# Performance work log

Measured on AMD Instinct MI355X. Metric: run time of the kernel, lower is better.

Reference implementation:

```python
import jax, jax.numpy as jnp
import numpy as np

B, T, C = 2, 4096, 2048
HS = 64          # module head size (r_k, kk normalize, GroupNorm groups)
H = C // HS      # 32
NK = 16          # kernel head dim (RUN_CUDA_RWKV7g views heads of 16)
HK = C // NK     # 128
LORA = 8
GN_EPS = 0.00064

def setup_inputs() -> dict:
    key = jax.random.key(0)
    ks = jax.random.split(key, 32)
    rn = lambda k, shape, s=1.0: jax.random.normal(k, shape, dtype=jnp.float32) * s
    sW = 0.5 / (C ** 0.5)
    return {
        'x': rn(ks[0], (B, T, C)),
        'v_first': rn(ks[1], (B, T, C)),
        'x_r': jax.random.uniform(ks[2], (1, 1, C)), 'x_w': jax.random.uniform(ks[3], (1, 1, C)),
        'x_k': jax.random.uniform(ks[4], (1, 1, C)), 'x_v': jax.random.uniform(ks[5], (1, 1, C)),
        'x_a': jax.random.uniform(ks[6], (1, 1, C)), 'x_g': jax.random.uniform(ks[7], (1, 1, C)),
        'w0': rn(ks[8], (1, 1, C), 0.5) - 3.0,
        'w1': rn(ks[9], (C, LORA), 0.02), 'w2': rn(ks[10], (LORA, C), 0.1),
        'a0': rn(ks[11], (1, 1, C), 0.1),
        'a1': rn(ks[12], (C, LORA), 0.02), 'a2': rn(ks[13], (LORA, C), 0.1),
        'v0': rn(ks[14], (1, 1, C), 0.1) + 0.73,
        'v1': rn(ks[15], (C, LORA), 0.02), 'v2': rn(ks[16], (LORA, C), 0.1),
        'g1': rn(ks[17], (C, LORA), 0.02), 'g2': rn(ks[18], (LORA, C), 0.1),
        'k_k': rn(ks[19], (1, 1, C), 0.05) + 0.71,
        'k_a': rn(ks[20], (1, 1, C), 0.05) + 1.02,
        'r_k': rn(ks[21], (H, HS), 0.02) - 0.04,
        'Wr': rn(ks[22], (C, C), sW), 'Wk': rn(ks[23], (C, C), 0.1 * sW),
        'Wv': rn(ks[24], (C, C), sW), 'Wo': rn(ks[25], (C, C), sW),
        'ln_g': jnp.ones((C,), jnp.float32), 'ln_b': jnp.zeros((C,), jnp.float32),
    }

def _rwkv7_scan(r, w, k, v, a, b):
    # each (B,T,C) -> heads (T,B,HK,NK); recurrence: S = S*exp(-exp(w)) + (S@a)b^T + v k^T; y = S@r
    th = lambda t: t.reshape(B, T, HK, NK).transpose(1, 0, 2, 3)
    rs, ws, ks_, vs, as_, bs = map(th, (r, w, k, v, a, b))
    decay = jnp.exp(-jnp.exp(ws))
    def step(S, inp):
        d_t, r_t, k_t, v_t, a_t, b_t = inp
        sa = jnp.einsum('bhij,bhj->bhi', S, a_t)                      # old state @ a
        S = (S * d_t[:, :, None, :]
             + sa[..., None] * b_t[:, :, None, :]
             + v_t[..., None] * k_t[:, :, None, :])
        y = jnp.einsum('bhij,bhj->bhi', S, r_t)
        return S, y
    S0 = jnp.zeros((B, HK, NK, NK), jnp.float32)
    _, ys = jax.lax.scan(step, S0, (decay, rs, ks_, vs, as_, bs))
    return ys.transpose(1, 0, 2, 3).reshape(B, T, C)

def reference(x, v_first, x_r, x_w, x_k, x_v, x_a, x_g,
              w0, w1, w2, a0, a1, a2, v0, v1, v2, g1, g2,
              k_k, k_a, r_k, Wr, Wk, Wv, Wo, ln_g, ln_b):
    xx = jnp.pad(x, ((0, 0), (1, 0), (0, 0)))[:, :T] - x   # token shift
    xr = x + xx * x_r; xw = x + xx * x_w; xk_ = x + xx * x_k
    xv = x + xx * x_v; xa = x + xx * x_a; xg_ = x + xx * x_g
    r = xr @ Wr.T
    w = -jax.nn.softplus(-(w0 + jnp.tanh(xw @ w1) @ w2)) - 0.5
    k = xk_ @ Wk.T
    v = xv @ Wv.T
    v_mix = jax.nn.sigmoid(v0 + (xv @ v1) @ v2)            # layer_id != 0 branch
    v = v + (v_first - v) * v_mix
    a = jax.nn.sigmoid(a0 + (xa @ a1) @ a2)
    g = jax.nn.sigmoid(xg_ @ g1) @ g2
    kk = k * k_k
    kk4 = kk.reshape(B, T, H, HS)
    kk = (kk4 / jnp.maximum(jnp.linalg.norm(kk4, axis=-1, keepdims=True), 1e-8)).reshape(B, T, C)
    k = k * (1 + (a - 1) * k_a)
    o = _rwkv7_scan(r, w, k, v, -kk, kk * a)
    # GroupNorm(H groups, eps=6.4e-4) over B*T rows
    og = o.reshape(B * T, H, HS)
    mu = og.mean(-1, keepdims=True)
    var = og.var(-1, keepdims=True)
    o = (((og - mu) / jnp.sqrt(var + GN_EPS)).reshape(B * T, C) * ln_g + ln_b).reshape(B, T, C)
    rh = r.reshape(B, T, H, HS); kh = k.reshape(B, T, H, HS); vh = v.reshape(B, T, H, HS)
    o = o + ((rh * kh * r_k).sum(-1, keepdims=True) * vh).reshape(B, T, C)
    out = (o * g) @ Wo.T
    return (out, v_first)
```

## Files before the change

### kernel.cpp

```cpp
#include <hip/hip_runtime.h>

#define T_LEN 4096
#define C_DIM 2048
#define REC 224
#define CH 64
#define CHB (CH * REC)

typedef __attribute__((ext_vector_type(4))) float f32x4;
typedef __attribute__((ext_vector_type(8))) __bf16 bf16x8;
typedef __attribute__((ext_vector_type(8))) unsigned short u16x8;
typedef __attribute__((ext_vector_type(4))) unsigned int u32x4;
typedef __attribute__((ext_vector_type(2))) unsigned int u32x2;
typedef unsigned short u16;
typedef unsigned int u32;

typedef __attribute__((address_space(1))) const void* as1cv;
typedef __attribute__((address_space(3))) void* as3v;

__device__ __forceinline__ void gld16(const void* g, void* l) {
  __builtin_amdgcn_global_load_lds((as1cv)g, (as3v)l, 16, 0, 0);
}

__device__ __forceinline__ u16 f2bf(float f) {
  union { float f; unsigned u; } x; x.f = f;
  return (u16)((x.u + 0x7fffu + ((x.u >> 16) & 1u)) >> 16);
}
__device__ __forceinline__ float bflo(unsigned u) {
  union { unsigned u; float f; } x; x.u = u << 16; return x.f;
}
__device__ __forceinline__ float bfhi(unsigned u) {
  union { unsigned u; float f; } x; x.u = u & 0xffff0000u; return x.f;
}
__device__ __forceinline__ float red16(float x) {
  int a;
  a = __builtin_amdgcn_update_dpp(0, __builtin_bit_cast(int, x), 0xB1, 0xF, 0xF, true);
  x += __builtin_bit_cast(float, a);
  a = __builtin_amdgcn_update_dpp(0, __builtin_bit_cast(int, x), 0x4E, 0xF, 0xF, true);
  x += __builtin_bit_cast(float, a);
  a = __builtin_amdgcn_update_dpp(0, __builtin_bit_cast(int, x), 0x124, 0xF, 0xF, true);
  x += __builtin_bit_cast(float, a);
  a = __builtin_amdgcn_update_dpp(0, __builtin_bit_cast(int, x), 0x128, 0xF, 0xF, true);
  x += __builtin_bit_cast(float, a);
  return x;
}
__device__ __forceinline__ f32x4 red16v(f32x4 v) {
  v[0] = red16(v[0]); v[1] = red16(v[1]);
  v[2] = red16(v[2]); v[3] = red16(v[3]);
  return v;
}

__global__ __launch_bounds__(256)
void conv_bf16_k(const float* __restrict__ s0, const float* __restrict__ s1,
                 const float* __restrict__ s2, const float* __restrict__ s3,
                 u16* __restrict__ d0) {
  const float* s = (blockIdx.y == 0) ? s0 : (blockIdx.y == 1) ? s1
                   : (blockIdx.y == 2) ? s2 : s3;
  u16* d = d0 + (size_t)blockIdx.y * 4194304;
  int i = (blockIdx.x * 256 + threadIdx.x) * 8;
  f32x4 a = *(const f32x4*)(s + i);
  f32x4 b = *(const f32x4*)(s + i + 4);
  u16x8 o;
  o[0] = f2bf(a[0]); o[1] = f2bf(a[1]); o[2] = f2bf(a[2]); o[3] = f2bf(a[3]);
  o[4] = f2bf(b[0]); o[5] = f2bf(b[1]); o[6] = f2bf(b[2]); o[7] = f2bf(b[3]);
  *(u16x8*)(d + i) = o;
}

__global__ __launch_bounds__(256)
void trans_lora_k(const float* __restrict__ w1, const float* __restrict__ a1,
                  const float* __restrict__ v1, const float* __restrict__ g1,
                  float* __restrict__ wt) {
  const float* s = (blockIdx.y == 0) ? w1 : (blockIdx.y == 1) ? a1
                   : (blockIdx.y == 2) ? v1 : g1;
  float* d = wt + (size_t)blockIdx.y * (8 * C_DIM);
  int c = blockIdx.x * 256 + threadIdx.x;
  f32x4 lo = *(const f32x4*)(s + c * 8);
  f32x4 hi = *(const f32x4*)(s + c * 8 + 4);
  d[0 * C_DIM + c] = lo[0]; d[1 * C_DIM + c] = lo[1];
  d[2 * C_DIM + c] = lo[2]; d[3 * C_DIM + c] = lo[3];
  d[4 * C_DIM + c] = hi[0]; d[5 * C_DIM + c] = hi[1];
  d[6 * C_DIM + c] = hi[2]; d[7 * C_DIM + c] = hi[3];
}

__global__ __launch_bounds__(256)
void mix_lora_k(const float* __restrict__ x,
                const float* __restrict__ xrw, const float* __restrict__ xww,
                const float* __restrict__ xkw, const float* __restrict__ xvw,
                const float* __restrict__ xaw, const float* __restrict__ xgw,
                const float* __restrict__ wt,
                u16* __restrict__ xr_bf, u16* __restrict__ xk_bf,
                u16* __restrict__ xv_bf, float* __restrict__ lora8) {
  const int pr = blockIdx.x * 2;
  const int t0 = pr & (T_LEN - 1);
  const int tid = threadIdx.x;
  const float* xr0 = x + (size_t)pr * C_DIM;
  const float* xr1 = xr0 + C_DIM;
  float wl0[8], al0[8], vl0[8], gl0[8];
  float wl1[8], al1[8], vl1[8], gl1[8];
  #pragma unroll
  for (int l = 0; l < 8; ++l) {
    wl0[l] = 0.f; al0[l] = 0.f; vl0[l] = 0.f; gl0[l] = 0.f;
    wl1[l] = 0.f; al1[l] = 0.f; vl1[l] = 0.f; gl1[l] = 0.f;
  }
  #pragma unroll
  for (int ii = 0; ii < 8; ++ii) {
    const int c = ii * 256 + tid;
    float x0 = xr0[c], x1 = xr1[c];
    float xm = t0 ? xr0[c - C_DIM] : 0.f;
    float dx0 = xm - x0;
    float dx1 = x0 - x1;
    float mr = xrw[c], mw = xww[c], mk = xkw[c];
    float mv = xvw[c], ma = xaw[c], mg = xgw[c];
    float xw0 = fmaf(dx0, mw, x0), xw1 = fmaf(dx1, mw, x1);
    float xa0 = fmaf(dx0, ma, x0), xa1 = fmaf(dx1, ma, x1);
    float xv0 = fmaf(dx0, mv, x0), xv1 = fmaf(dx1, mv, x1);
    float xg0 = fmaf(dx0, mg, x0), xg1 = fmaf(dx1, mg, x1);
    xr_bf[(size_t)pr * C_DIM + c] = f2bf(fmaf(dx0, mr, x0));
    xr_bf[(size_t)(pr + 1) * C_DIM + c] = f2bf(fmaf(dx1, mr, x1));
    xk_bf[(size_t)pr * C_DIM + c] = f2bf(fmaf(dx0, mk, x0));
    xk_bf[(size_t)(pr + 1) * C_DIM + c] = f2bf(fmaf(dx1, mk, x1));
    xv_bf[(size_t)pr * C_DIM + c] = f2bf(xv0);
    xv_bf[(size_t)(pr + 1) * C_DIM + c] = f2bf(xv1);
    #pragma unroll
    for (int l = 0; l < 8; ++l) {
      float tw = wt[l * C_DIM + c];
      float ta = wt[16384 + l * C_DIM + c];
      float tv = wt[32768 + l * C_DIM + c];
      float tg = wt[49152 + l * C_DIM + c];
      wl0[l] = fmaf(xw0, tw, wl0[l]); wl1[l] = fmaf(xw1, tw, wl1[l]);
      al0[l] = fmaf(xa0, ta, al0[l]); al1[l] = fmaf(xa1, ta, al1[l]);
      vl0[l] = fmaf(xv0, tv, vl0[l]); vl1[l] = fmaf(xv1, tv, vl1[l]);
      gl0[l] = fmaf(xg0, tg, gl0[l]); gl1[l] = fmaf(xg1, tg, gl1[l]);
    }
  }
  __shared__ __attribute__((aligned(16))) float red2[2][16][32];
  const int row = tid >> 4;
  f32x4 t0v, t1v;
  #pragma unroll
  for (int half = 0; half < 2; ++half) {
    float* wl = half ? wl1 : wl0;
    float* al = half ? al1 : al0;
    float* vl = half ? vl1 : vl0;
    float* gl = half ? gl1 : gl0;
    t0v = red16v((f32x4){wl[0], wl[1], wl[2], wl[3]});
    t1v = red16v((f32x4){wl[4], wl[5], wl[6], wl[7]});
    if ((tid & 15) == 0) {
      *(f32x4*)&red2[half][row][0] = t0v; *(f32x4*)&red2[half][row][4] = t1v;
    }
    t0v = red16v((f32x4){al[0], al[1], al[2], al[3]});
    t1v = red16v((f32x4){al[4], al[5], al[6], al[7]});
    if ((tid & 15) == 0) {
      *(f32x4*)&red2[half][row][8] = t0v; *(f32x4*)&red2[half][row][12] = t1v;
    }
    t0v = red16v((f32x4){vl[0], vl[1], vl[2], vl[3]});
    t1v = red16v((f32x4){vl[4], vl[5], vl[6], vl[7]});
    if ((tid & 15) == 0) {
      *(f32x4*)&red2[half][row][16] = t0v; *(f32x4*)&red2[half][row][20] = t1v;
    }
    t0v = red16v((f32x4){gl[0], gl[1], gl[2], gl[3]});
    t1v = red16v((f32x4){gl[4], gl[5], gl[6], gl[7]});
    if ((tid & 15) == 0) {
      *(f32x4*)&red2[half][row][24] = t0v; *(f32x4*)&red2[half][row][28] = t1v;
    }
  }
  __syncthreads();
  if (tid < 64) {
    const int rw = tid >> 5, idx = tid & 31;
    float s = 0.f;
    #pragma unroll
    for (int r = 0; r < 16; ++r) s += red2[rw][r][idx];
    int mat = idx >> 3;
    if (mat == 0) s = tanhf(s);
    else if (mat == 3) s = 1.f / (1.f + expf(-s));
    lora8[(size_t)(pr + rw) * 32 + idx] = s;
  }
}

__device__ __forceinline__ int swzslot(int row, int slot) {
  return slot ^ ((row >> 1) & 3);
}

__global__ __launch_bounds__(512)
void gemm8_k(const u16* __restrict__ A0, const u16* __restrict__ A1,
             const u16* __restrict__ A2, const u16* __restrict__ B0,
             const u16* __restrict__ B1, const u16* __restrict__ B2,
             char* __restrict__ out, int pmode) {
  extern __shared__ __attribute__((aligned(16))) char smem[];
  u16* Asm = (u16*)smem;
  u16* Bsm = (u16*)(smem + 65536);
  const int z = blockIdx.z;
  const u16* A = (z == 0) ? A0 : (z == 1) ? A1 : A2;
  const u16* Bw = (z == 0) ? B0 : (z == 1) ? B1 : B2;
  const int sbase = (z == 0) ? 4 : (z == 1) ? 6 : 192;
  const int sstr = (z == 2) ? 2 : 8;
  const int tid = threadIdx.x;
  const int wv = tid >> 6, ln = tid & 63;
  const int wr = wv >> 2, wc = wv & 3;
  const int bid = blockIdx.x + (blockIdx.y << 3);
  const int sw = (bid & 7) * 32 + (bid >> 3);
  const int row0 = (sw >> 3) * 256, col0 = (sw & 7) * 256;
  const int s_rw = tid >> 2;
  const int s_slotL = (tid & 3) ^ ((s_rw >> 1) & 3);
  int aoff[8], boff[4];
  #pragma unroll
  for (int m = 0; m < 8; ++m) {
    int row = wr * 128 + m * 16 + (ln & 15);
    aoff[m] = row * 32 + swzslot(row, ln >> 4) * 8;
  }
  #pragma unroll
  for (int n = 0; n < 4; ++n) {
    int row = wc * 64 + n * 16 + (ln & 15);
    boff[n] = row * 32 + swzslot(row, ln >> 4) * 8;
  }
  f32x4 acc[8][4];
  #pragma unroll
  for (int m = 0; m < 8; ++m)
    #pragma unroll
    for (int n = 0; n < 4; ++n) acc[m][n] = (f32x4){0.f, 0.f, 0.f, 0.f};

  auto abase = [&](int db, int kh) -> u16* { return Asm + (db * 2 + kh) * 8192; };
  auto bbase = [&](int db, int kh) -> u16* { return Bsm + (db * 2 + kh) * 8192; };
  auto stage1 = [&](const u16* src, int baserow, u16* lbase, int kh, int skt, int rblk) {
    const u16* g = src + (size_t)(baserow + rblk * 128 + s_rw) * 2048
                   + skt * 64 + kh * 32 + s_slotL * 8;
    gld16(g, lbase + rblk * 4096 + wv * 512);
  };
  auto khblockA = [&](int db, int skt, bool doStage) {
    const u16* Ab = abase(db, 0);
    const u16* Bb = bbase(db, 0);
    const int sdb = skt & 1;
    bf16x8 bf[4], af[4];
    #pragma unroll
    for (int n = 0; n < 4; ++n) bf[n] = *(const bf16x8*)(Bb + boff[n]);
    #pragma unroll
    for (int m = 0; m < 4; ++m) af[m] = *(const bf16x8*)(Ab + aoff[m]);
    if (doStage) {
      stage1(A, row0, abase(sdb, 0), 0, skt, 0);
      stage1(A, row0, abase(sdb, 0), 0, skt, 1);
      stage1(Bw, col0, bbase(sdb, 0), 0, skt, 0);
      stage1(Bw, col0, bbase(sdb, 0), 0, skt, 1);
    }
    __builtin_amdgcn_s_setprio(1);
    #pragma unroll
    for (int m = 0; m < 4; ++m)
      #pragma unroll
      for (int n = 0; n < 4; ++n)
        acc[m][n] = __builtin_amdgcn_mfma_f32_16x16x32_bf16(af[m], bf[n], acc[m][n], 0, 0, 0);
    __builtin_amdgcn_s_setprio(0);
    #pragma unroll
    for (int m = 0; m < 4; ++m) af[m] = *(const bf16x8*)(Ab + aoff[4 + m]);
    if (doStage) {
      stage1(A, row0, abase(sdb, 1), 1, skt, 0);
      stage1(A, row0, abase(sdb, 1), 1, skt, 1);
      stage1(Bw, col0, bbase(sdb, 1), 1, skt, 0);
      stage1(Bw, col0, bbase(sdb, 1), 1, skt, 1);
    }
    __builtin_amdgcn_s_setprio(1);
    #pragma unroll
    for (int m = 0; m < 4; ++m)
      #pragma unroll
      for (int n = 0; n < 4; ++n)
        acc[4 + m][n] = __builtin_amdgcn_mfma_f32_16x16x32_bf16(af[m], bf[n], acc[4 + m][n], 0, 0, 0);
    __builtin_amdgcn_s_setprio(0);
  };
  auto khblockB = [&](int db) {
    const u16* Ab = abase(db, 1);
    const u16* Bb = bbase(db, 1);
    bf16x8 bf[4], af[4];
    #pragma unroll
    for (int n = 0; n < 4; ++n) bf[n] = *(const bf16x8*)(Bb + boff[n]);
    #pragma unroll
    for (int m = 0; m < 4; ++m) af[m] = *(const bf16x8*)(Ab + aoff[m]);
    __builtin_amdgcn_s_setprio(1);
    #pragma unroll
    for (int m = 0; m < 4; ++m)
      #pragma unroll
      for (int n = 0; n < 4; ++n)
        acc[m][n] = __builtin_amdgcn_mfma_f32_16x16x32_bf16(af[m], bf[n], acc[m][n], 0, 0, 0);
    __builtin_amdgcn_s_setprio(0);
    #pragma unroll
    for (int m = 0; m < 4; ++m) af[m] = *(const bf16x8*)(Ab + aoff[4 + m]);
    __builtin_amdgcn_s_setprio(1);
    #pragma unroll
    for (int m = 0; m < 4; ++m)
      #pragma unroll
      for (int n = 0; n < 4; ++n)
        acc[4 + m][n] = __builtin_amdgcn_mfma_f32_16x16x32_bf16(af[m], bf[n], acc[4 + m][n], 0, 0, 0);
    __builtin_amdgcn_s_setprio(0);
  };

  stage1(A, row0, abase(0, 0), 0, 0, 0); stage1(A, row0, abase(0, 0), 0, 0, 1);
  stage1(Bw, col0, bbase(0, 0), 0, 0, 0); stage1(Bw, col0, bbase(0, 0), 0, 0, 1);
  stage1(A, row0, abase(0, 1), 1, 0, 0); stage1(A, row0, abase(0, 1), 1, 0, 1);
  stage1(Bw, col0, bbase(0, 1), 1, 0, 0); stage1(Bw, col0, bbase(0, 1), 1, 0, 1);
  asm volatile("s_waitcnt vmcnt(4)" ::: "memory");
  __builtin_amdgcn_s_barrier();
  for (int kt = 0; kt < 32; ++kt) {
    const int db = kt & 1;
    khblockA(db, kt + 1, kt < 31);
    if (kt < 31) asm volatile("s_waitcnt vmcnt(8)" ::: "memory");
    else         asm volatile("s_waitcnt vmcnt(0)" ::: "memory");
    __builtin_amdgcn_s_barrier();
    khblockB(db);
    if (kt < 31) {
      asm volatile("s_waitcnt vmcnt(4)" ::: "memory");
      __builtin_amdgcn_s_barrier();
    }
  }

  const int rowb = row0 + wr * 128 + ((ln >> 4) << 2);
  const int colb = col0 + wc * 64 + (ln & 15);
  #pragma unroll
  for (int m = 0; m < 8; ++m)
    #pragma unroll
    for (int n = 0; n < 4; ++n)
      #pragma unroll
      for (int qq = 0; qq < 4; ++qq) {
        int row = rowb + m * 16 + qq;
        int col = colb + n * 16;
        float val = acc[m][n][qq];
        if (pmode == 0) {
          ((float*)out)[(size_t)row * 2048 + col] = val;
        } else {
          int bq = row >> 12, tq = row & (T_LEN - 1);
          int hq = col >> 4, jq = col & 15;
          *(u16*)(out + (size_t)((bq * 128 + hq) * T_LEN + tq) * REC
                  + sbase + jq * sstr) = f2bf(val);
        }
      }
}

__global__ __launch_bounds__(256)
void post_gemm_k(const float* __restrict__ v_first, const float* __restrict__ lora8,
                 const float* __restrict__ w0, const float* __restrict__ w2,
                 const float* __restrict__ a0, const float* __restrict__ a2,
                 const float* __restrict__ v0, const float* __restrict__ v2,
                 const float* __restrict__ k_k, const float* __restrict__ k_a,
                 char* __restrict__ packed) {
  const int tg = blockIdx.x;
  const int mo = blockIdx.y;
  const int bq = blockIdx.z;
  const int tid = threadIdx.x;
  const int wv = tid >> 6, ln = tid & 63;
  const int t = tg * 4 + wv;
  const int cc = ln & 15;
  const int hq = mo * 4 + (ln >> 4);
  const int c = mo * 64 + ln;
  char* pb = packed + (size_t)((bq * 128 + hq) * T_LEN + t) * REC;
  const int rr = bq * T_LEN + t;
  u32 kr = *(const u32*)(pb + cc * 8 + 4);
  float kraw = bflo(kr);
  float vraw = bflo(*(const u16*)(pb + 192 + cc * 2));
  float vf = v_first[(size_t)rr * C_DIM + c];
  const float* lo = lora8 + (size_t)rr * 32;
  float wr_ = w0[c], ar_ = a0[c], vr_ = v0[c];
  #pragma unroll
  for (int l = 0; l < 8; ++l) {
    wr_ = fmaf(lo[l], w2[l * C_DIM + c], wr_);
    ar_ = fmaf(lo[8 + l], a2[l * C_DIM + c], ar_);
    vr_ = fmaf(lo[16 + l], v2[l * C_DIM + c], vr_);
  }
  float w_ = -log1pf(expf(-wr_)) - 0.5f;
  float dec = expf(-expf(w_));
  float a_ = 1.f / (1.f + expf(-ar_));
  float vm = 1.f / (1.f + expf(-vr_));
  float vnew = fmaf(vf - vraw, vm, vraw);
  float kk = kraw * k_k[c];
  float ss = red16(kk * kk);
  ss += __shfl_xor(ss, 16);
  ss += __shfl_xor(ss, 32);
  float sc = 1.f / fmaxf(sqrtf(ss), 1e-8f);
  float kn = kk * sc;
  u16 wa = f2bf(-kn);
  u16 wb = f2bf(kn * a_);
  u16 wk = f2bf(kraw * fmaf(a_ - 1.f, k_a[c], 1.f));
  *(u32*)(pb + cc * 8) = (u32)wa | ((u32)wb << 16);
  *(u32*)(pb + cc * 8 + 4) = (u32)wk | (kr & 0xffff0000u);
  *(u16*)(pb + 192 + cc * 2) = f2bf(vnew);
  *(float*)(pb + 128 + cc * 4) = dec;
}

__device__ __forceinline__ void stage(const char* g, char* l, int wv, int ln) {
  gld16(g + wv * 1024 + ln * 16, l + wv * 1024);
  gld16(g + 4096 + wv * 1024 + ln * 16, l + 4096 + wv * 1024);
  gld16(g + 8192 + wv * 1024 + ln * 16, l + 8192 + wv * 1024);
  if (wv < 2) gld16(g + 12288 + wv * 1024 + ln * 16, l + 12288 + wv * 1024);
}

__global__ __launch_bounds__(256)
void scan_k(char* __restrict__ packed) {
  __shared__ __attribute__((aligned(16))) char bufm[2 * CHB + 1024];
  __shared__ __attribute__((aligned(16))) float ybuf[CH * 16];
  const int hb = blockIdx.x;
  const int tid = threadIdx.x;
  const int wv = tid >> 6, ln = tid & 63;
  const int j = ln & 15;
  const int i = wv * 4 + (ln >> 4);
  char* src = packed + (size_t)hb * (T_LEN * REC);
  float S = 0.f;
  stage(src, bufm, wv, ln);
  const int NC = T_LEN / CH;
  for (int c = 0; c < NC; ++c) {
    asm volatile("s_waitcnt vmcnt(0)" ::: "memory");
    __syncthreads();
    if (c + 1 < NC)
      stage(src + (size_t)(c + 1) * CHB, bufm + ((c + 1) & 1) * CHB, wv, ln);
    const char* Bp = bufm + (c & 1) * CHB;
    const char* p0 = Bp + j * 8;
    const char* pd = Bp + 128 + j * 4;
    const char* pv = Bp + 192 + i * 2;
    u32x2 kq[4]; float dq[4]; u32 vq[4];
    #pragma unroll
    for (int s = 0; s < 4; ++s) {
      kq[s] = *(const u32x2*)(p0 + s * REC);
      dq[s] = *(const float*)(pd + s * REC);
      vq[s] = *(const u16*)(pv + s * REC);
    }
    float yq0 = 0.f, yq1 = 0.f, yq2 = 0.f, yq3 = 0.f;
    #pragma unroll
    for (int t = 0; t < CH; ++t) {
      const int st = t & 3;
      u32x2 kc = kq[st]; float dc = dq[st]; u32 vc = vq[st];
      kq[st] = *(const u32x2*)(p0 + (t + 4) * REC);
      dq[st] = *(const float*)(pd + (t + 4) * REC);
      vq[st] = *(const u16*)(pv + (t + 4) * REC);
      float a_ = bflo(kc[0]), b_ = bfhi(kc[0]);
      float k_ = bflo(kc[1]), r_ = bfhi(kc[1]);
      float v_ = bflo(vc);
      float sa = red16(S * a_);
      S = fmaf(S, dc, fmaf(sa, b_, v_ * k_));
      float yv = red16(S * r_);
      const bool own = (j == (t & 15));
      if ((t >> 4) == 0)      yq0 = own ? yv : yq0;
      else if ((t >> 4) == 1) yq1 = own ? yv : yq1;
      else if ((t >> 4) == 2) yq2 = own ? yv : yq2;
      else                    yq3 = own ? yv : yq3;
    }
    ybuf[(0 * 16 + j) * 16 + i] = yq0;
    ybuf[(1 * 16 + j) * 16 + i] = yq1;
    ybuf[(2 * 16 + j) * 16 + i] = yq2;
    ybuf[(3 * 16 + j) * 16 + i] = yq3;
    __syncthreads();
    {
      const int rec = tid >> 2, part = tid & 3;
      f32x4 y4 = *(const f32x4*)(ybuf + rec * 16 + part * 4);
      *(f32x4*)(src + (size_t)c * CHB + rec * REC + 128 + part * 16) = y4;
    }
  }
}

__global__ __launch_bounds__(256)
void post_gn_k(const char* __restrict__ packed, const float* __restrict__ lora8,
               const float* __restrict__ g2, const float* __restrict__ ln_g,
               const float* __restrict__ ln_b, const float* __restrict__ r_k,
               u16* __restrict__ og) {
  const int tg = blockIdx.x;
  const int mo = blockIdx.y;
  const int bq = blockIdx.z;
  const int tid = threadIdx.x;
  const int wv = tid >> 6, ln = tid & 63;
  const int t = tg * 4 + wv;
  const int cc = ln & 15;
  const int hq = mo * 4 + (ln >> 4);
  const int c = mo * 64 + ln;
  const char* pb = packed + (size_t)((bq * 128 + hq) * T_LEN + t) * REC;
  u32 kr = *(const u32*)(pb + cc * 8 + 4);
  float kv = bflo(kr), rv = bfhi(kr);
  float vv = bflo(*(const u16*)(pb + 192 + cc * 2));
  float o = *(const float*)(pb + 128 + cc * 4);
  const int rr = bq * T_LEN + t;
  const float* lo = lora8 + (size_t)rr * 32 + 24;
  float gg = 0.f;
  #pragma unroll
  for (int l = 0; l < 8; ++l) gg = fmaf(lo[l], g2[l * C_DIM + c], gg);
  float s1 = red16(o);
  float s2 = red16(o * o);
  float srk = red16(rv * kv * r_k[c]);
  s1 += __shfl_xor(s1, 16); s2 += __shfl_xor(s2, 16); srk += __shfl_xor(srk, 16);
  s1 += __shfl_xor(s1, 32); s2 += __shfl_xor(s2, 32); srk += __shfl_xor(srk, 32);
  float mu = s1 * (1.f / 64.f);
  float var = s2 * (1.f / 64.f) - mu * mu;
  float rstd = rsqrtf(var + 0.00064f);
  float on = fmaf((o - mu) * rstd, ln_g[c], ln_b[c]);
  float o2 = fmaf(srk, vv, on);
  og[(size_t)rr * C_DIM + c] = f2bf(o2 * gg);
}

extern "C" void kernel_launch(void* const* d_in, const int* in_sizes, int n_in,
                              void* d_out, int out_size, void* d_ws, size_t ws_size,
                              hipStream_t stream) {
  (void)in_sizes; (void)n_in; (void)out_size;
  const float* x      = (const float*)d_in[0];
  const float* v_first= (const float*)d_in[1];
  const float* x_r    = (const float*)d_in[2];
  const float* x_w    = (const float*)d_in[3];
  const float* x_k    = (const float*)d_in[4];
  const float* x_v    = (const float*)d_in[5];
  const float* x_a    = (const float*)d_in[6];
  const float* x_g    = (const float*)d_in[7];
  const float* w0     = (const float*)d_in[8];
  const float* w1     = (const float*)d_in[9];
  const float* w2     = (const float*)d_in[10];
  const float* a0     = (const float*)d_in[11];
  const float* a1     = (const float*)d_in[12];
  const float* a2     = (const float*)d_in[13];
  const float* v0     = (const float*)d_in[14];
  const float* v1     = (const float*)d_in[15];
  const float* v2     = (const float*)d_in[16];
  const float* g1     = (const float*)d_in[17];
  const float* g2     = (const float*)d_in[18];
  const float* k_k    = (const float*)d_in[19];
  const float* k_a    = (const float*)d_in[20];
  const float* r_k    = (const float*)d_in[21];
  const float* Wr     = (const float*)d_in[22];
  const float* Wk     = (const float*)d_in[23];
  const float* Wv     = (const float*)d_in[24];
  const float* Wo     = (const float*)d_in[25];
  const float* ln_g   = (const float*)d_in[26];
  const float* ln_b   = (const float*)d_in[27];

  if (ws_size < 370147328ull) return;
  char* ws = (char*)d_ws;
  u16* Wr_bf = (u16*)(ws + 0);
  u16* Wk_bf = Wr_bf + 4194304;
  u16* Wv_bf = Wk_bf + 4194304;
  u16* Wo_bf = Wv_bf + 4194304;
  u16* xr_bf = (u16*)(ws + 33554432);
  u16* xk_bf = xr_bf + 16777216;
  u16* xv_bf = xk_bf + 16777216;
  float* lora8 = (float*)(ws + 134217728);
  char* packed = ws + 135266304;
  float* wt = (float*)packed;
  u16* og = xr_bf;
  float* out = (float*)d_out;

  (void)hipFuncSetAttribute((const void*)gemm8_k,
                            hipFuncAttributeMaxDynamicSharedMemorySize, 131072);

  conv_bf16_k<<<dim3(2048, 4), 256, 0, stream>>>(Wr, Wk, Wv, Wo, Wr_bf);
  trans_lora_k<<<dim3(8, 4), 256, 0, stream>>>(w1, a1, v1, g1, wt);

  mix_lora_k<<<4096, 256, 0, stream>>>(x, x_r, x_w, x_k, x_v, x_a, x_g,
                                       wt, xr_bf, xk_bf, xv_bf, lora8);

  gemm8_k<<<dim3(8, 32, 3), 512, 131072, stream>>>(xk_bf, xr_bf, xv_bf,
                                                   Wk_bf, Wr_bf, Wv_bf,
                                                   packed, 1);

  post_gemm_k<<<dim3(1024, 32, 2), 256, 0, stream>>>(v_first, lora8, w0, w2,
                                                     a0, a2, v0, v2,
                                                     k_k, k_a, packed);

  scan_k<<<256, 256, 0, stream>>>(packed);

  post_gn_k<<<dim3(1024, 32, 2), 256, 0, stream>>>(packed, lora8, g2,
                                                   ln_g, ln_b, r_k, og);

  gemm8_k<<<dim3(8, 32, 1), 512, 131072, stream>>>(og, og, og,
                                                   Wo_bf, Wo_bf, Wo_bf,
                                                   (char*)out, 0);

  hipMemcpyAsync(out + 16777216, v_first, (size_t)16777216 * 4,
                 hipMemcpyDeviceToDevice, stream);
}
```

Measured before the change: 1.129 ms.

## Restructure GEMM mainloop into triple-buffered K=32 stages with split A/B prefetch

Replaces the double-buffered K=64 (two half-steps) GEMM pipeline with a three-slot ring of K=32 stages, prefetching two stages ahead, with A and B loads issued in separate halves of each iteration. LDS use drops from 128KB to 96KB per block. The aim is a deeper prefetch and fewer waits per MFMA. The cost is an extra barrier per iteration and twice as many loop iterations.

```diff
diff --git a/kernel.cpp b/kernel.cpp
--- a/kernel.cpp
+++ b/kernel.cpp
@@ -185,8 +185,6 @@
              const u16* __restrict__ B1, const u16* __restrict__ B2,
              char* __restrict__ out, int pmode) {
   extern __shared__ __attribute__((aligned(16))) char smem[];
-  u16* Asm = (u16*)smem;
-  u16* Bsm = (u16*)(smem + 65536);
   const int z = blockIdx.z;
   const u16* A = (z == 0) ? A0 : (z == 1) ? A1 : A2;
   const u16* Bw = (z == 0) ? B0 : (z == 1) ? B1 : B2;
@@ -217,28 +215,35 @@
     #pragma unroll
     for (int n = 0; n < 4; ++n) acc[m][n] = (f32x4){0.f, 0.f, 0.f, 0.f};
 
-  auto abase = [&](int db, int kh) -> u16* { return Asm + (db * 2 + kh) * 8192; };
-  auto bbase = [&](int db, int kh) -> u16* { return Bsm + (db * 2 + kh) * 8192; };
-  auto stage1 = [&](const u16* src, int baserow, u16* lbase, int kh, int skt, int rblk) {
-    const u16* g = src + (size_t)(baserow + rblk * 128 + s_rw) * 2048
-                   + skt * 64 + kh * 32 + s_slotL * 8;
-    gld16(g, lbase + rblk * 4096 + wv * 512);
+  auto bufA = [&](int b) -> u16* { return (u16*)smem + b * 16384; };
+  auto bufB = [&](int b) -> u16* { return (u16*)smem + b * 16384 + 8192; };
+  auto stageA = [&](int kt, int b, int rblk) {
+    const u16* g = A + (size_t)(row0 + rblk * 128 + s_rw) * 2048 + kt * 32 + s_slotL * 8;
+    gld16(g, bufA(b) + rblk * 4096 + wv * 512);
   };
-  auto khblockA = [&](int db, int skt, bool doStage) {
-    const u16* Ab = abase(db, 0);
-    const u16* Bb = bbase(db, 0);
-    const int sdb = skt & 1;
+  auto stageB = [&](int kt, int b, int rblk) {
+    const u16* g = Bw + (size_t)(col0 + rblk * 128 + s_rw) * 2048 + kt * 32 + s_slotL * 8;
+    gld16(g, bufB(b) + rblk * 4096 + wv * 512);
+  };
+
+  stageA(0, 0, 0); stageA(0, 0, 1); stageB(0, 0, 0); stageB(0, 0, 1);
+  stageA(1, 1, 0); stageA(1, 1, 1); stageB(1, 1, 0); stageB(1, 1, 1);
+
+  int b = 0;
+  for (int kt = 0; kt < 64; ++kt) {
+    if (kt < 63) asm volatile("s_waitcnt vmcnt(4)" ::: "memory");
+    else         asm volatile("s_waitcnt vmcnt(0)" ::: "memory");
+    __builtin_amdgcn_s_barrier();
+    const u16* Ab = bufA(b);
+    const u16* Bb = bufB(b);
+    int b2 = b + 2; if (b2 >= 3) b2 -= 3;
+    const bool st = (kt + 2) < 64;
     bf16x8 bf[4], af[4];
     #pragma unroll
     for (int n = 0; n < 4; ++n) bf[n] = *(const bf16x8*)(Bb + boff[n]);
     #pragma unroll
     for (int m = 0; m < 4; ++m) af[m] = *(const bf16x8*)(Ab + aoff[m]);
-    if (doStage) {
-      stage1(A, row0, abase(sdb, 0), 0, skt, 0);
-      stage1(A, row0, abase(sdb, 0), 0, skt, 1);
-      stage1(Bw, col0, bbase(sdb, 0), 0, skt, 0);
-      stage1(Bw, col0, bbase(sdb, 0), 0, skt, 1);
-    }
+    if (st) { stageA(kt + 2, b2, 0); stageA(kt + 2, b2, 1); }
     __builtin_amdgcn_s_setprio(1);
     #pragma unroll
     for (int m = 0; m < 4; ++m)
@@ -246,14 +251,10 @@
       for (int n = 0; n < 4; ++n)
         acc[m][n] = __builtin_amdgcn_mfma_f32_16x16x32_bf16(af[m], bf[n], acc[m][n], 0, 0, 0);
     __builtin_amdgcn_s_setprio(0);
+    __builtin_amdgcn_s_barrier();
     #pragma unroll
     for (int m = 0; m < 4; ++m) af[m] = *(const bf16x8*)(Ab + aoff[4 + m]);
-    if (doStage) {
-      stage1(A, row0, abase(sdb, 1), 1, skt, 0);
-      stage1(A, row0, abase(sdb, 1), 1, skt, 1);
-      stage1(Bw, col0, bbase(sdb, 1), 1, skt, 0);
-      stage1(Bw, col0, bbase(sdb, 1), 1, skt, 1);
-    }
+    if (st) { stageB(kt + 2, b2, 0); stageB(kt + 2, b2, 1); }
     __builtin_amdgcn_s_setprio(1);
     #pragma unroll
     for (int m = 0; m < 4; ++m)
@@ -261,50 +262,7 @@
       for (int n = 0; n < 4; ++n)
         acc[4 + m][n] = __builtin_amdgcn_mfma_f32_16x16x32_bf16(af[m], bf[n], acc[4 + m][n], 0, 0, 0);
     __builtin_amdgcn_s_setprio(0);
-  };
-  auto khblockB = [&](int db) {
-    const u16* Ab = abase(db, 1);
-    const u16* Bb = bbase(db, 1);
-    bf16x8 bf[4], af[4];
-    #pragma unroll
-    for (int n = 0; n < 4; ++n) bf[n] = *(const bf16x8*)(Bb + boff[n]);
-    #pragma unroll
-    for (int m = 0; m < 4; ++m) af[m] = *(const bf16x8*)(Ab + aoff[m]);
-    __builtin_amdgcn_s_setprio(1);
-    #pragma unroll
-    for (int m = 0; m < 4; ++m)
-      #pragma unroll
-      for (int n = 0; n < 4; ++n)
-        acc[m][n] = __builtin_amdgcn_mfma_f32_16x16x32_bf16(af[m], bf[n], acc[m][n], 0, 0, 0);
-    __builtin_amdgcn_s_setprio(0);
-    #pragma unroll
-    for (int m = 0; m < 4; ++m) af[m] = *(const bf16x8*)(Ab + aoff[4 + m]);
-    __builtin_amdgcn_s_setprio(1);
-    #pragma unroll
-    for (int m = 0; m < 4; ++m)
-      #pragma unroll
-      for (int n = 0; n < 4; ++n)
-        acc[4 + m][n] = __builtin_amdgcn_mfma_f32_16x16x32_bf16(af[m], bf[n], acc[4 + m][n], 0, 0, 0);
-    __builtin_amdgcn_s_setprio(0);
-  };
-
-  stage1(A, row0, abase(0, 0), 0, 0, 0); stage1(A, row0, abase(0, 0), 0, 0, 1);
-  stage1(Bw, col0, bbase(0, 0), 0, 0, 0); stage1(Bw, col0, bbase(0, 0), 0, 0, 1);
-  stage1(A, row0, abase(0, 1), 1, 0, 0); stage1(A, row0, abase(0, 1), 1, 0, 1);
-  stage1(Bw, col0, bbase(0, 1), 1, 0, 0); stage1(Bw, col0, bbase(0, 1), 1, 0, 1);
-  asm volatile("s_waitcnt vmcnt(4)" ::: "memory");
-  __builtin_amdgcn_s_barrier();
-  for (int kt = 0; kt < 32; ++kt) {
-    const int db = kt & 1;
-    khblockA(db, kt + 1, kt < 31);
-    if (kt < 31) asm volatile("s_waitcnt vmcnt(8)" ::: "memory");
-    else         asm volatile("s_waitcnt vmcnt(0)" ::: "memory");
-    __builtin_amdgcn_s_barrier();
-    khblockB(db);
-    if (kt < 31) {
-      asm volatile("s_waitcnt vmcnt(4)" ::: "memory");
-      __builtin_amdgcn_s_barrier();
-    }
+    b = (b + 1 == 3) ? 0 : b + 1;
   }
 
   const int rowb = row0 + wr * 128 + ((ln >> 4) << 2);
@@ -534,7 +492,7 @@
   float* out = (float*)d_out;
 
   (void)hipFuncSetAttribute((const void*)gemm8_k,
-                            hipFuncAttributeMaxDynamicSharedMemorySize, 131072);
+                            hipFuncAttributeMaxDynamicSharedMemorySize, 98304);
 
   conv_bf16_k<<<dim3(2048, 4), 256, 0, stream>>>(Wr, Wk, Wv, Wo, Wr_bf);
   trans_lora_k<<<dim3(8, 4), 256, 0, stream>>>(w1, a1, v1, g1, wt);
@@ -542,9 +500,9 @@
   mix_lora_k<<<4096, 256, 0, stream>>>(x, x_r, x_w, x_k, x_v, x_a, x_g,
                                        wt, xr_bf, xk_bf, xv_bf, lora8);
 
-  gemm8_k<<<dim3(8, 32, 3), 512, 131072, stream>>>(xk_bf, xr_bf, xv_bf,
-                                                   Wk_bf, Wr_bf, Wv_bf,
-                                                   packed, 1);
+  gemm8_k<<<dim3(8, 32, 3), 512, 98304, stream>>>(xk_bf, xr_bf, xv_bf,
+                                                  Wk_bf, Wr_bf, Wv_bf,
+                                                  packed, 1);
 
   post_gemm_k<<<dim3(1024, 32, 2), 256, 0, stream>>>(v_first, lora8, w0, w2,
                                                      a0, a2, v0, v2,
@@ -555,9 +513,9 @@
   post_gn_k<<<dim3(1024, 32, 2), 256, 0, stream>>>(packed, lora8, g2,
                                                    ln_g, ln_b, r_k, og);
 
-  gemm8_k<<<dim3(8, 32, 1), 512, 131072, stream>>>(og, og, og,
-                                                   Wo_bf, Wo_bf, Wo_bf,
-                                                   (char*)out, 0);
+  gemm8_k<<<dim3(8, 32, 1), 512, 98304, stream>>>(og, og, og,
+                                                  Wo_bf, Wo_bf, Wo_bf,
+                                                  (char*)out, 0);
 
   hipMemcpyAsync(out + 16777216, v_first, (size_t)16777216 * 4,
                  hipMemcpyDeviceToDevice, stream);
```

After: 1.082 ms. 4.2% less time.
